# Performance work log

Hardware: AMD Instinct MI355X
Metric: run time of the kernel (lower is better)

Reference implementation:

```python
import jax, jax.numpy as jnp
import numpy as np

B, D, S = 4, 512, 2048
H, DK = 8, 64  # d_model = H * DK
SCALE = float(np.sqrt(DK))
EPS = 1e-8


def setup_inputs() -> dict:
    key = jax.random.key(0)
    ks = jax.random.split(key, 9)
    std = (2.0 / D) ** 0.5  # kaiming_normal fan_out for 1x1 conv
    inp = {"x": jax.random.normal(ks[0], (B, D, 2, S), dtype=jnp.float32)}
    i = 1
    for n in ("q", "k", "v", "o"):
        inp[f"W{n}_r"] = jax.random.normal(ks[i], (D, D), dtype=jnp.float32) * std
        inp[f"W{n}_i"] = jax.random.normal(ks[i + 1], (D, D), dtype=jnp.float32) * std
        inp[f"b{n}_r"] = jnp.zeros((D,), dtype=jnp.float32)
        inp[f"b{n}_i"] = jnp.zeros((D,), dtype=jnp.float32)
        i += 2
    return inp


def _cconv(x, Wr, Wi, br, bi):
    # complex 1x1 conv: x [B, D, 2, S] -> [B, D, 2, S]
    real, imag = x[:, :, 0, :], x[:, :, 1, :]
    o_r = (jnp.einsum('od,bds->bos', Wr, real)
           - jnp.einsum('od,bds->bos', Wi, imag) + (br - bi)[None, :, None])
    o_i = (jnp.einsum('od,bds->bos', Wr, imag)
           + jnp.einsum('od,bds->bos', Wi, real) + (br + bi)[None, :, None])
    return jnp.stack([o_r, o_i], axis=2)


def reference(x, Wq_r, Wq_i, bq_r, bq_i, Wk_r, Wk_i, bk_r, bk_i,
              Wv_r, Wv_i, bv_r, bv_i, Wo_r, Wo_i, bo_r, bo_i):
    b, c, _, s = x.shape
    Q = _cconv(x, Wq_r, Wq_i, bq_r, bq_i).reshape(b, H, DK, 2, s)
    K = _cconv(x, Wk_r, Wk_i, bk_r, bk_i).reshape(b, H, DK, 2, s)
    V = _cconv(x, Wv_r, Wv_i, bv_r, bv_i).reshape(b, H, DK, 2, s)
    Qm = jnp.sqrt(Q[:, :, :, 0] ** 2 + Q[:, :, :, 1] ** 2 + EPS)  # [b,H,DK,s]
    Km = jnp.sqrt(K[:, :, :, 0] ** 2 + K[:, :, :, 1] ** 2 + EPS)
    scores = jnp.einsum('bhds,bhdt->bhst', Qm, Km) / SCALE  # [b,H,s,s]
    attn = jax.nn.softmax(scores, axis=-1)  # dropout is identity in eval
    Vr = jnp.einsum('bhst,bhdt->bhds', attn, V[:, :, :, 0])  # [b,H,DK,s]
    Vi = jnp.einsum('bhst,bhdt->bhds', attn, V[:, :, :, 1])
    out = jnp.stack([Vr.reshape(b, c, s), Vi.reshape(b, c, s)], axis=2)
    return _cconv(out, Wo_r, Wo_i, bo_r, bo_i)
```

## Files before the change

kernel.cpp:

```cpp
#include <hip/hip_runtime.h>
#include <math.h>
#include <stdint.h>

typedef __attribute__((ext_vector_type(8))) _Float16 f16x8;
typedef __attribute__((ext_vector_type(2))) __fp16 fp16x2;
typedef __attribute__((ext_vector_type(4))) float f32x4;
typedef __attribute__((ext_vector_type(16))) float f32x16;

static __device__ __forceinline__ unsigned short f2h(float f) {
  union { _Float16 h; unsigned short u; } v; v.h = (_Float16)f;
  return v.u;
}
static __device__ __forceinline__ float h2f(unsigned short u) {
  union { unsigned short u; _Float16 h; } v; v.u = u;
  return (float)v.h;
}
static __device__ __forceinline__ unsigned pkrtz(float a, float b) {
  union { fp16x2 h; unsigned u; } v;
  v.h = __builtin_amdgcn_cvt_pkrtz(a, b);
  return v.u;
}

#define GLOAD_LDS16(g, l) __builtin_amdgcn_global_load_lds( \
    (const __attribute__((address_space(1))) void*)(g),     \
    (__attribute__((address_space(3))) void*)(l), 16, 0, 0)

__global__ __launch_bounds__(256) void pack_w4(
    const float* __restrict__ Wr0, const float* __restrict__ Wi0,
    const float* __restrict__ br0, const float* __restrict__ bi0,
    const float* __restrict__ Wr1, const float* __restrict__ Wi1,
    const float* __restrict__ br1, const float* __restrict__ bi1,
    const float* __restrict__ Wr2, const float* __restrict__ Wi2,
    const float* __restrict__ br2, const float* __restrict__ bi2,
    const float* __restrict__ Wr3, const float* __restrict__ Wi3,
    const float* __restrict__ br3, const float* __restrict__ bi3,
    unsigned short* __restrict__ W2, float* __restrict__ bias2) {
  const int s = blockIdx.y;
  const float* Wr = (s == 0) ? Wr0 : (s == 1) ? Wr1 : (s == 2) ? Wr2 : Wr3;
  const float* Wi = (s == 0) ? Wi0 : (s == 1) ? Wi1 : (s == 2) ? Wi2 : Wi3;
  const float* br = (s == 0) ? br0 : (s == 1) ? br1 : (s == 2) ? br2 : br3;
  const float* bi = (s == 0) ? bi0 : (s == 1) ? bi1 : (s == 2) ? bi2 : bi3;
  W2 += (size_t)s * 1024 * 1024;
  bias2 += s * 1024;
  int idx = blockIdx.x * 256 + threadIdx.x;
  int m = idx >> 10, k = idx & 1023;
  int o = m & 511, d = k & 511;
  float v;
  if (m < 512) v = (k < 512) ? Wr[o * 512 + d] : -Wi[o * 512 + d];
  else         v = (k < 512) ? Wi[o * 512 + d] :  Wr[o * 512 + d];
  W2[idx] = f2h(v);
  if (idx < 1024) {
    int oo = idx & 511;
    bias2[idx] = (idx < 512) ? (br[oo] - bi[oo]) : (br[oo] + bi[oo]);
  }
}

__global__ __launch_bounds__(256) void pack_x(
    const float* __restrict__ x, unsigned short* __restrict__ XT) {
  __shared__ unsigned short tl[64][72];
  const int t = threadIdx.x;
  const int sBase = blockIdx.x * 64, dBase = blockIdx.y * 64;
  const int b = blockIdx.z >> 1, c = blockIdx.z & 1;
  const int r = t >> 2, cb = (t & 3) * 16;
  const float* src = x + (((size_t)(b * 512 + dBase + r) * 2 + c) * 2048 + sBase + cb);
#pragma unroll
  for (int j = 0; j < 16; j += 4) {
    float4 v = *(const float4*)(src + j);
    tl[cb + j + 0][r] = f2h(v.x);
    tl[cb + j + 1][r] = f2h(v.y);
    tl[cb + j + 2][r] = f2h(v.z);
    tl[cb + j + 3][r] = f2h(v.w);
  }
  __syncthreads();
  const int s = t >> 2, dc = (t & 3) * 16;
  unsigned short* dst = XT + ((size_t)(b * 2048 + sBase + s)) * 1024 + c * 512 + dBase + dc;
  *(uint4*)dst = *(const uint4*)&tl[s][dc];
  *(uint4*)(dst + 8) = *(const uint4*)&tl[s][dc + 8];
}

template <int MODE>
__global__ __launch_bounds__(256) void gemm_bt(
    const unsigned short* __restrict__ A, const unsigned short* __restrict__ Bt,
    const float* __restrict__ bias, unsigned short* __restrict__ Cb,
    float* __restrict__ Cf) {
  __shared__ unsigned short As[128 * 32];
  __shared__ unsigned short Bs[128 * 32];
  const int t = threadIdx.x;
  const int wave = t >> 6, lane = t & 63;
  const int wr = wave >> 1, wc = wave & 1;
  const int bid = blockIdx.x;
  const int xcd = bid & 7, g = bid >> 3;
  const int i = g & 63, z = g >> 6;
  const int nb = xcd * 8 + (i >> 3), mb = i & 7;
  const int mBase = mb * 128, nBase = nb * 128;
  A += (size_t)z * 1024 * 1024;
  bias += z * 1024;
  if (MODE == 0) Cb += (size_t)z * 1024 * 8192;
  const int lr = lane & 15, lk = (lane >> 4) * 8;
  f32x4 acc[4][4] = {};
  const int grow = wave * 32 + (lane >> 2);
  const int gcol = (lane & 3) * 8;
  const unsigned short* ga = A + (size_t)(mBase + grow) * 1024 + gcol;
  const unsigned short* gb = Bt + (size_t)(nBase + grow) * 1024 + gcol;
  unsigned short* lA = &As[wave * 1024];
  unsigned short* lB = &Bs[wave * 1024];
  for (int k0 = 0; k0 < 1024; k0 += 32) {
    __syncthreads();
    GLOAD_LDS16(ga + k0, lA);
    GLOAD_LDS16(ga + 16 * 1024 + k0, lA + 512);
    GLOAD_LDS16(gb + k0, lB);
    GLOAD_LDS16(gb + 16 * 1024 + k0, lB + 512);
    __syncthreads();
    f16x8 af[4], bfr[4];
#pragma unroll
    for (int i2 = 0; i2 < 4; ++i2) {
      af[i2]  = *(const f16x8*)&As[(wr * 64 + i2 * 16 + lr) * 32 + lk];
      bfr[i2] = *(const f16x8*)&Bs[(wc * 64 + i2 * 16 + lr) * 32 + lk];
    }
#pragma unroll
    for (int i2 = 0; i2 < 4; ++i2)
#pragma unroll
      for (int j = 0; j < 4; ++j)
        acc[i2][j] = __builtin_amdgcn_mfma_f32_16x16x32_f16(af[i2], bfr[j], acc[i2][j], 0, 0, 0);
  }
  const int cr = (lane >> 4) * 4, cc = lane & 15;
#pragma unroll
  for (int i2 = 0; i2 < 4; ++i2) {
#pragma unroll
    for (int j = 0; j < 4; ++j) {
      const int m0 = mBase + wr * 64 + i2 * 16 + cr;
      const int n0 = nBase + wc * 64 + j * 16 + cc;
#pragma unroll
      for (int g2 = 0; g2 < 4; ++g2) {
        float v = acc[i2][j][g2] + bias[m0 + g2];
        if (MODE == 0) {
          const int m = m0 + g2;
          if (z == 2) {
            const int ri = m >> 9, mm = m & 511;
            const int h = mm >> 6, dloc = mm & 63;
            const int jj = dloc >> 5, q31 = dloc & 31;
            const int b = n0 >> 11, s = n0 & 2047;
            const int tile = s >> 6, ks = (s >> 4) & 3, hi = (s >> 3) & 1, e = s & 7;
            const size_t flat =
                ((((((size_t)(b * 8 + h) * 32 + tile) * 4 + ks) * 2 + jj) * 2 + ri) * 64 +
                 hi * 32 + q31) * 8 + e;
            Cb[flat] = f2h(v);
          } else {
            Cb[(size_t)m * 8192 + n0] = f2h(v);
          }
        } else {
          const int m = m0 + g2;
          const int c = m >> 9, o = m & 511;
          const int b = n0 >> 11, s = n0 & 2047;
          Cf[(size_t)b * 2097152 + (size_t)o * 4096 + c * 2048 + s] = v;
        }
      }
    }
  }
}

__global__ __launch_bounds__(256) void mag_qk(
    const unsigned short* __restrict__ Cq, const unsigned short* __restrict__ Ck,
    unsigned short* __restrict__ Qm, unsigned short* __restrict__ Km) {
  __shared__ unsigned short tl[64][72];
  const int isK = blockIdx.z;
  const unsigned short* C = isK ? Ck : Cq;
  unsigned short* Out = isK ? Km : Qm;
  const int t = threadIdx.x;
  const int sBase = blockIdx.x * 64;
  const int bh = blockIdx.y, b = bh >> 3, h = bh & 7;
  const int d = t >> 2, sc = (t & 3) * 16;
  const unsigned short* pr = C + (size_t)(h * 64 + d) * 8192 + b * 2048 + sBase + sc;
  const unsigned short* pi = pr + (size_t)512 * 8192;
  unsigned short rb[16], ib[16];
  *(uint4*)&rb[0] = *(const uint4*)pr;  *(uint4*)&rb[8] = *(const uint4*)(pr + 8);
  *(uint4*)&ib[0] = *(const uint4*)pi;  *(uint4*)&ib[8] = *(const uint4*)(pi + 8);
#pragma unroll
  for (int j = 0; j < 16; ++j) {
    float fr = h2f(rb[j]), fi = h2f(ib[j]);
    tl[sc + j][d] = f2h(sqrtf(fr * fr + fi * fi + 1e-8f));
  }
  __syncthreads();
  const int s = t >> 2, dc = (t & 3) * 16;
  if (isK) {
    const int kb = s >> 5, q31 = s & 31, db = dc >> 4;
    unsigned short* dstf = Out +
        ((((size_t)bh * 32 + blockIdx.x) * 2 + kb) * 4 + db) * 512 + (size_t)q31 * 8;
    *(uint4*)dstf = *(const uint4*)&tl[s][dc];
    *(uint4*)(dstf + 256) = *(const uint4*)&tl[s][dc + 8];
  } else {
    unsigned short* dst = Out + ((size_t)bh * 2048 + sBase + s) * 64 + dc;
    *(uint4*)dst = *(const uint4*)&tl[s][dc];
    *(uint4*)(dst + 8) = *(const uint4*)&tl[s][dc + 8];
  }
}

__global__ __launch_bounds__(256) void attn(
    const unsigned short* __restrict__ Qm, const unsigned short* __restrict__ Km,
    const unsigned short* __restrict__ Vf, unsigned short* __restrict__ OutT) {
  const int t = threadIdx.x, wave = t >> 6, lane = t & 63;
  const int id = blockIdx.x;
  const int xcd = id & 7, within = id >> 3;
  const int bh = xcd * 4 + (within >> 4);
  const int qtile = within & 15;
  const int b = bh >> 3, h = bh & 7;
  const int q31 = lane & 31, hi = lane >> 5;
  const int qBase = qtile * 128 + wave * 32;
  const float ls = 0.18033688f;

  f16x8 qf[4];
  {
    const unsigned short* qp = Qm + ((size_t)bh * 2048 + qBase + q31) * 64 + hi * 8;
    qf[0] = *(const f16x8*)qp;
    qf[1] = *(const f16x8*)(qp + 16);
    qf[2] = *(const f16x8*)(qp + 32);
    qf[3] = *(const f16x8*)(qp + 48);
  }
  f32x16 Or[2] = {}, Oi[2] = {};
  float m = -1e30f, l = 0.f;

  const unsigned short* kmF = Km + (size_t)bh * 131072 + (size_t)lane * 8;
  const unsigned short* vF  = Vf + (size_t)bh * 262144 + (size_t)lane * 8;

  for (int t0 = 0; t0 < 2048; t0 += 64) {
    const int tile = t0 >> 6;
    f16x8 kf[2][4];
#pragma unroll
    for (int kb = 0; kb < 2; ++kb)
#pragma unroll
      for (int db = 0; db < 4; ++db)
        kf[kb][db] = *(const f16x8*)(kmF + (size_t)(((tile * 2 + kb) * 4 + db)) * 512);
    __builtin_amdgcn_sched_barrier(0);
    f32x16 S[2] = {};
#pragma unroll
    for (int kb = 0; kb < 2; ++kb)
#pragma unroll
      for (int db = 0; db < 4; ++db)
        S[kb] = __builtin_amdgcn_mfma_f32_32x32x16_f16(kf[kb][db], qf[db], S[kb], 0, 0, 0);
    f16x8 vr[4][2], vi[4][2];
#pragma unroll
    for (int ks = 0; ks < 4; ++ks)
#pragma unroll
      for (int j = 0; j < 2; ++j) {
        const size_t u = (size_t)(((tile * 4 + ks) * 2 + j) * 2) * 512;
        vr[ks][j] = *(const f16x8*)(vF + u);
        vi[ks][j] = *(const f16x8*)(vF + u + 512);
      }
    __builtin_amdgcn_sched_barrier(0);
    float m0a = fmaxf(S[0][0], S[0][1]), m0b = fmaxf(S[0][2], S[0][3]);
#pragma unroll
    for (int r = 4; r < 16; r += 4) {
      m0a = fmaxf(m0a, fmaxf(S[0][r], S[0][r + 1]));
      m0b = fmaxf(m0b, fmaxf(S[0][r + 2], S[0][r + 3]));
    }
#pragma unroll
    for (int r = 0; r < 16; r += 4) {
      m0a = fmaxf(m0a, fmaxf(S[1][r], S[1][r + 1]));
      m0b = fmaxf(m0b, fmaxf(S[1][r + 2], S[1][r + 3]));
    }
    float vmax = fmaxf(m0a, m0b);
    vmax = fmaxf(vmax, __shfl_xor(vmax, 32, 64));
    float pmax = vmax * ls;
    if (__any(pmax > m + 8.0f)) {
      float mnew = fmaxf(m, pmax);
      float al = __builtin_amdgcn_exp2f(m - mnew);
      m = mnew;
      l *= al;
#pragma unroll
      for (int r = 0; r < 16; ++r) {
        const int qloc = (r & 3) + 8 * (r >> 2) + 4 * hi;
        float ao = __shfl(al, qloc, 64);
        Or[0][r] *= ao; Or[1][r] *= ao;
        Oi[0][r] *= ao; Oi[1][r] *= ao;
      }
    }
    float p[2][16];
    float ps0 = 0.f, ps1 = 0.f;
#pragma unroll
    for (int kb = 0; kb < 2; ++kb)
#pragma unroll
      for (int r = 0; r < 16; r += 2) {
        float pa_ = __builtin_amdgcn_exp2f(fmaf(S[kb][r], ls, -m));
        float pb_ = __builtin_amdgcn_exp2f(fmaf(S[kb][r + 1], ls, -m));
        p[kb][r] = pa_; p[kb][r + 1] = pb_;
        ps0 += pa_; ps1 += pb_;
      }
    float ps = ps0 + ps1;
    ps += __shfl_xor(ps, 32, 64);
    l += ps;
    f16x8 pa[4];
#pragma unroll
    for (int ks = 0; ks < 4; ++ks) {
      const float* pp = &p[ks >> 1][8 * (ks & 1)];
      unsigned c0 = pkrtz(pp[0], pp[1]);
      unsigned c1 = pkrtz(pp[2], pp[3]);
      unsigned d0 = pkrtz(pp[4], pp[5]);
      unsigned d1 = pkrtz(pp[6], pp[7]);
      asm volatile("v_permlane32_swap_b32 %0, %1" : "+v"(c0), "+v"(d0));
      asm volatile("v_permlane32_swap_b32 %0, %1" : "+v"(c1), "+v"(d1));
      union { unsigned u[4]; f16x8 v; } w;
      w.u[0] = c0; w.u[1] = c1; w.u[2] = d0; w.u[3] = d1;
      pa[ks] = w.v;
    }
#pragma unroll
    for (int ks = 0; ks < 4; ++ks)
#pragma unroll
      for (int j = 0; j < 2; ++j) {
        Or[j] = __builtin_amdgcn_mfma_f32_32x32x16_f16(pa[ks], vr[ks][j], Or[j], 0, 0, 0);
        Oi[j] = __builtin_amdgcn_mfma_f32_32x32x16_f16(pa[ks], vi[ks][j], Oi[j], 0, 0, 0);
      }
  }
  float linv = 1.0f / l;
#pragma unroll
  for (int r = 0; r < 16; ++r) {
    const int qloc = (r & 3) + 8 * (r >> 2) + 4 * hi;
    float iv = __shfl(linv, qloc, 64);
    unsigned short* orow = OutT + ((size_t)b * 2048 + qBase + qloc) * 1024 + h * 64;
    orow[q31]       = f2h(Or[0][r] * iv);
    orow[32 + q31]  = f2h(Or[1][r] * iv);
    orow[512 + q31] = f2h(Oi[0][r] * iv);
    orow[544 + q31] = f2h(Oi[1][r] * iv);
  }
}

extern "C" void kernel_launch(void* const* d_in, const int* in_sizes, int n_in,
                              void* d_out, int out_size, void* d_ws, size_t ws_size,
                              hipStream_t stream) {
  (void)in_sizes; (void)n_in; (void)out_size; (void)ws_size;
  const float* x = (const float*)d_in[0];

  unsigned short* XT = (unsigned short*)d_ws;
  unsigned short* W2 = XT + (size_t)8192 * 1024;
  float* bias2 = (float*)(W2 + (size_t)4 * 1024 * 1024);
  unsigned short* Cqkv = (unsigned short*)(bias2 + 4096);
  unsigned short* Qm = (unsigned short*)d_out;
  unsigned short* Km = Qm + (size_t)4 * 8 * 2048 * 64;
  unsigned short* Vf = Cqkv + (size_t)2 * 1024 * 8192;
  unsigned short* OutT = Cqkv;

  pack_w4<<<dim3(4096, 4), 256, 0, stream>>>(
      (const float*)d_in[1],  (const float*)d_in[2],  (const float*)d_in[3],  (const float*)d_in[4],
      (const float*)d_in[5],  (const float*)d_in[6],  (const float*)d_in[7],  (const float*)d_in[8],
      (const float*)d_in[9],  (const float*)d_in[10], (const float*)d_in[11], (const float*)d_in[12],
      (const float*)d_in[13], (const float*)d_in[14], (const float*)d_in[15], (const float*)d_in[16],
      W2, bias2);
  pack_x<<<dim3(32, 8, 8), 256, 0, stream>>>(x, XT);
  gemm_bt<0><<<1536, 256, 0, stream>>>(W2, XT, bias2, Cqkv, nullptr);
  mag_qk<<<dim3(32, 32, 2), 256, 0, stream>>>(Cqkv, Cqkv + (size_t)1024 * 8192, Qm, Km);
  attn<<<512, 256, 0, stream>>>(Qm, Km, Vf, OutT);
  gemm_bt<1><<<512, 256, 0, stream>>>(
      W2 + (size_t)3 * 1024 * 1024, OutT, bias2 + 3 * 1024, nullptr, (float*)d_out);
}
```

Measured before the change: 206.4 us.

## Fuse Q/K magnitude computation into projection GEMM epilogue

```diff
diff --git a/kernel.cpp b/kernel.cpp
--- a/kernel.cpp
+++ b/kernel.cpp
@@ -81,8 +81,9 @@
 template <int MODE>
 __global__ __launch_bounds__(256) void gemm_bt(
     const unsigned short* __restrict__ A, const unsigned short* __restrict__ Bt,
-    const float* __restrict__ bias, unsigned short* __restrict__ Cb,
-    float* __restrict__ Cf) {
+    const float* __restrict__ bias,
+    unsigned short* __restrict__ Qo, unsigned short* __restrict__ Ko,
+    unsigned short* __restrict__ Vo, float* __restrict__ Cf) {
   __shared__ unsigned short As[128 * 32];
   __shared__ unsigned short Bs[128 * 32];
   const int t = threadIdx.x;
@@ -92,22 +93,28 @@
   const int xcd = bid & 7, g = bid >> 3;
   const int i = g & 63, z = g >> 6;
   const int nb = xcd * 8 + (i >> 3), mb = i & 7;
-  const int mBase = mb * 128, nBase = nb * 128;
+  const int nBase = nb * 128;
   A += (size_t)z * 1024 * 1024;
   bias += z * 1024;
-  if (MODE == 0) Cb += (size_t)z * 1024 * 8192;
   const int lr = lane & 15, lk = (lane >> 4) * 8;
   f32x4 acc[4][4] = {};
-  const int grow = wave * 32 + (lane >> 2);
   const int gcol = (lane & 3) * 8;
-  const unsigned short* ga = A + (size_t)(mBase + grow) * 1024 + gcol;
-  const unsigned short* gb = Bt + (size_t)(nBase + grow) * 1024 + gcol;
+  const unsigned short* ga;
+  size_t gaStep;
+  if (MODE == 0 && z < 2) {
+    ga = A + (size_t)(mb * 64 + wave * 16 + (lane >> 2)) * 1024 + gcol;
+    gaStep = (size_t)512 * 1024;
+  } else {
+    ga = A + (size_t)(mb * 128 + wave * 32 + (lane >> 2)) * 1024 + gcol;
+    gaStep = (size_t)16 * 1024;
+  }
+  const unsigned short* gb = Bt + (size_t)(nBase + wave * 32 + (lane >> 2)) * 1024 + gcol;
   unsigned short* lA = &As[wave * 1024];
   unsigned short* lB = &Bs[wave * 1024];
   for (int k0 = 0; k0 < 1024; k0 += 32) {
     __syncthreads();
     GLOAD_LDS16(ga + k0, lA);
-    GLOAD_LDS16(ga + 16 * 1024 + k0, lA + 512);
+    GLOAD_LDS16(ga + gaStep + k0, lA + 512);
     GLOAD_LDS16(gb + k0, lB);
     GLOAD_LDS16(gb + 16 * 1024 + k0, lB + 512);
     __syncthreads();
@@ -124,18 +131,46 @@
         acc[i2][j] = __builtin_amdgcn_mfma_f32_16x16x32_f16(af[i2], bfr[j], acc[i2][j], 0, 0, 0);
   }
   const int cr = (lane >> 4) * 4, cc = lane & 15;
-#pragma unroll
-  for (int i2 = 0; i2 < 4; ++i2) {
-#pragma unroll
-    for (int j = 0; j < 4; ++j) {
-      const int m0 = mBase + wr * 64 + i2 * 16 + cr;
-      const int n0 = nBase + wc * 64 + j * 16 + cc;
-#pragma unroll
-      for (int g2 = 0; g2 < 4; ++g2) {
-        float v = acc[i2][j][g2] + bias[m0 + g2];
-        if (MODE == 0) {
-          const int m = m0 + g2;
-          if (z == 2) {
+  if (MODE == 0 && z < 2) {
+    unsigned short* Out = (z == 0) ? Qo : Ko;
+    const int ob = mb * 64 + wr * 32;
+#pragma unroll
+    for (int u = 0; u < 2; ++u) {
+#pragma unroll
+      for (int j = 0; j < 4; ++j) {
+        const int n0 = nBase + wc * 64 + j * 16 + cc;
+        const int bq = n0 >> 11, ss = n0 & 2047;
+#pragma unroll
+        for (int g2 = 0; g2 < 4; ++g2) {
+          const int o = ob + u * 16 + cr + g2;
+          float vr_ = acc[2 * u][j][g2] + bias[o];
+          float vi_ = acc[2 * u + 1][j][g2] + bias[512 + o];
+          float mag = sqrtf(vr_ * vr_ + vi_ * vi_ + 1e-8f);
+          const int hh = o >> 6, dl = o & 63;
+          const int bh = bq * 8 + hh;
+          if (z == 0) {
+            Out[((size_t)bh * 2048 + ss) * 64 + dl] = f2h(mag);
+          } else {
+            const size_t flat =
+                ((((size_t)bh * 32 + (ss >> 6)) * 2 + ((ss >> 5) & 1)) * 4 + (dl >> 4)) * 512 +
+                ((dl >> 3) & 1) * 256 + (ss & 31) * 8 + (dl & 7);
+            Out[flat] = f2h(mag);
+          }
+        }
+      }
+    }
+  } else {
+#pragma unroll
+    for (int i2 = 0; i2 < 4; ++i2) {
+#pragma unroll
+      for (int j = 0; j < 4; ++j) {
+        const int m0 = mb * 128 + wr * 64 + i2 * 16 + cr;
+        const int n0 = nBase + wc * 64 + j * 16 + cc;
+#pragma unroll
+        for (int g2 = 0; g2 < 4; ++g2) {
+          float v = acc[i2][j][g2] + bias[m0 + g2];
+          if (MODE == 0) {
+            const int m = m0 + g2;
             const int ri = m >> 9, mm = m & 511;
             const int h = mm >> 6, dloc = mm & 63;
             const int jj = dloc >> 5, q31 = dloc & 31;
@@ -144,54 +179,16 @@
             const size_t flat =
                 ((((((size_t)(b * 8 + h) * 32 + tile) * 4 + ks) * 2 + jj) * 2 + ri) * 64 +
                  hi * 32 + q31) * 8 + e;
-            Cb[flat] = f2h(v);
+            Vo[flat] = f2h(v);
           } else {
-            Cb[(size_t)m * 8192 + n0] = f2h(v);
+            const int m = m0 + g2;
+            const int c = m >> 9, o = m & 511;
+            const int b = n0 >> 11, s = n0 & 2047;
+            Cf[(size_t)b * 2097152 + (size_t)o * 4096 + c * 2048 + s] = v;
           }
-        } else {
-          const int m = m0 + g2;
-          const int c = m >> 9, o = m & 511;
-          const int b = n0 >> 11, s = n0 & 2047;
-          Cf[(size_t)b * 2097152 + (size_t)o * 4096 + c * 2048 + s] = v;
         }
       }
     }
-  }
-}
-
-__global__ __launch_bounds__(256) void mag_qk(
-    const unsigned short* __restrict__ Cq, const unsigned short* __restrict__ Ck,
-    unsigned short* __restrict__ Qm, unsigned short* __restrict__ Km) {
-  __shared__ unsigned short tl[64][72];
-  const int isK = blockIdx.z;
-  const unsigned short* C = isK ? Ck : Cq;
-  unsigned short* Out = isK ? Km : Qm;
-  const int t = threadIdx.x;
-  const int sBase = blockIdx.x * 64;
-  const int bh = blockIdx.y, b = bh >> 3, h = bh & 7;
-  const int d = t >> 2, sc = (t & 3) * 16;
-  const unsigned short* pr = C + (size_t)(h * 64 + d) * 8192 + b * 2048 + sBase + sc;
-  const unsigned short* pi = pr + (size_t)512 * 8192;
-  unsigned short rb[16], ib[16];
-  *(uint4*)&rb[0] = *(const uint4*)pr;  *(uint4*)&rb[8] = *(const uint4*)(pr + 8);
-  *(uint4*)&ib[0] = *(const uint4*)pi;  *(uint4*)&ib[8] = *(const uint4*)(pi + 8);
-#pragma unroll
-  for (int j = 0; j < 16; ++j) {
-    float fr = h2f(rb[j]), fi = h2f(ib[j]);
-    tl[sc + j][d] = f2h(sqrtf(fr * fr + fi * fi + 1e-8f));
-  }
-  __syncthreads();
-  const int s = t >> 2, dc = (t & 3) * 16;
-  if (isK) {
-    const int kb = s >> 5, q31 = s & 31, db = dc >> 4;
-    unsigned short* dstf = Out +
-        ((((size_t)bh * 32 + blockIdx.x) * 2 + kb) * 4 + db) * 512 + (size_t)q31 * 8;
-    *(uint4*)dstf = *(const uint4*)&tl[s][dc];
-    *(uint4*)(dstf + 256) = *(const uint4*)&tl[s][dc + 8];
-  } else {
-    unsigned short* dst = Out + ((size_t)bh * 2048 + sBase + s) * 64 + dc;
-    *(uint4*)dst = *(const uint4*)&tl[s][dc];
-    *(uint4*)(dst + 8) = *(const uint4*)&tl[s][dc + 8];
   }
 }
 
@@ -345,9 +342,9 @@
       (const float*)d_in[13], (const float*)d_in[14], (const float*)d_in[15], (const float*)d_in[16],
       W2, bias2);
   pack_x<<<dim3(32, 8, 8), 256, 0, stream>>>(x, XT);
-  gemm_bt<0><<<1536, 256, 0, stream>>>(W2, XT, bias2, Cqkv, nullptr);
-  mag_qk<<<dim3(32, 32, 2), 256, 0, stream>>>(Cqkv, Cqkv + (size_t)1024 * 8192, Qm, Km);
+  gemm_bt<0><<<1536, 256, 0, stream>>>(W2, XT, bias2, Qm, Km, Vf, nullptr);
   attn<<<512, 256, 0, stream>>>(Qm, Km, Vf, OutT);
   gemm_bt<1><<<512, 256, 0, stream>>>(
-      W2 + (size_t)3 * 1024 * 1024, OutT, bias2 + 3 * 1024, nullptr, (float*)d_out);
-}
+      W2 + (size_t)3 * 1024 * 1024, OutT, bias2 + 3 * 1024, nullptr, nullptr, nullptr,
+      (float*)d_out);
+}
```

New measurement: 209.2 us. Within noise of the previous version (+1.3%).
